# Kernel tuning notes

Measured on AMD Instinct MI355X. Metric: run time of the kernel, lower is better.

Reference implementation:

```python
import jax, jax.numpy as jnp
import numpy as np

B, T, C = 2, 2048, 1024
N_HEAD = 16
HEAD_DIM = C // N_HEAD


def setup_inputs() -> dict:
    key = jax.random.key(0)
    k1, k2, k3, k4, k5 = jax.random.split(key, 5)
    s = 1.0 / np.sqrt(C)
    return {
        "x": jax.random.normal(k1, (B, T, C), dtype=jnp.float32),
        "w_attn": jax.random.normal(k2, (C, 3 * C), dtype=jnp.float32) * s,
        "b_attn": jax.random.normal(k3, (3 * C,), dtype=jnp.float32) * 0.02,
        "w_proj": jax.random.normal(k4, (C, C), dtype=jnp.float32) * s,
        "b_proj": jax.random.normal(k5, (C,), dtype=jnp.float32) * 0.02,
    }


def reference(x, w_attn, b_attn, w_proj, b_proj):
    Bx, Tx, Cx = x.shape
    qkv = x @ w_attn + b_attn  # [B, T, 3C]
    q, k, v = jnp.split(qkv, 3, axis=2)
    # [B, H, T, D]
    q = q.reshape(Bx, Tx, N_HEAD, HEAD_DIM).transpose(0, 2, 1, 3)
    k = k.reshape(Bx, Tx, N_HEAD, HEAD_DIM).transpose(0, 2, 1, 3)
    v = v.reshape(Bx, Tx, N_HEAD, HEAD_DIM).transpose(0, 2, 1, 3)
    scale = 1.0 / jnp.sqrt(jnp.asarray(HEAD_DIM, dtype=x.dtype))
    att = jnp.einsum("bhqd,bhkd->bhqk", q, k) * scale  # [B,H,T,T]
    causal = jnp.tril(jnp.ones((Tx, Tx), dtype=bool))
    att = jnp.where(causal[None, None, :, :], att, -jnp.inf)
    att = jax.nn.softmax(att, axis=-1)
    y = jnp.einsum("bhqk,bhkd->bhqd", att, v)  # [B,H,T,D]
    y = y.transpose(0, 2, 1, 3).reshape(Bx, Tx, Cx)
    return y @ w_proj + b_proj
```

## Files before the change

### kernel.cpp

```cpp
#include <hip/hip_runtime.h>
#include <hip/hip_bf16.h>
#include <stdint.h>

#define TT 2048
#define CC 1024
#define NH 16
#define HD 64
#define BT 4096

typedef float f32x4 __attribute__((ext_vector_type(4)));
typedef __bf16 bf16x8 __attribute__((ext_vector_type(8)));
typedef __bf16 bf16x4 __attribute__((ext_vector_type(4)));

#define MFMA(a, b, c) __builtin_amdgcn_mfma_f32_16x16x32_bf16((a), (b), (c), 0, 0, 0)

__device__ __forceinline__ void gload16(const void* g, void* l) {
    __builtin_amdgcn_global_load_lds(
        (const __attribute__((address_space(1))) void*)g,
        (__attribute__((address_space(3))) void*)l,
        16, 0, 0);
}

__global__ __launch_bounds__(256) void conv_f32_bf16(
    const float* __restrict__ in, __bf16* __restrict__ out, int n4) {
    int i = blockIdx.x * blockDim.x + threadIdx.x;
    int stride = gridDim.x * blockDim.x;
    for (; i < n4; i += stride) {
        float4 v = reinterpret_cast<const float4*>(in)[i];
        bf16x4 o;
        o.x = (__bf16)v.x; o.y = (__bf16)v.y; o.z = (__bf16)v.z; o.w = (__bf16)v.w;
        reinterpret_cast<bf16x4*>(out)[i] = o;
    }
}

__global__ __launch_bounds__(256) void transpose_f32_bf16(
    const float* __restrict__ in, __bf16* __restrict__ out, int R, int C) {
    __shared__ float tile[32][33];
    int c0 = blockIdx.x * 32, r0 = blockIdx.y * 32;
    int tx = threadIdx.x, ty = threadIdx.y;
#pragma unroll
    for (int j = 0; j < 32; j += 8)
        tile[ty + j][tx] = in[(size_t)(r0 + ty + j) * C + c0 + tx];
    __syncthreads();
#pragma unroll
    for (int j = 0; j < 32; j += 8)
        out[(size_t)(c0 + ty + j) * R + r0 + tx] = (__bf16)tile[tx][ty + j];
}

template <int MODE>
__global__ __launch_bounds__(256) void gemm128(
    const __bf16* __restrict__ A, const __bf16* __restrict__ Bt,
    const float* __restrict__ bias,
    __bf16* __restrict__ oq, __bf16* __restrict__ ok, __bf16* __restrict__ ov,
    float* __restrict__ of, int M, int N, int K) {
    __shared__ __align__(16) __bf16 As[128 * 64];
    __shared__ __align__(16) __bf16 Bs[128 * 64];
    const int tid = threadIdx.x;
    const int w = tid >> 6, lane = tid & 63;
    const int l15 = lane & 15, lg = lane >> 4;
    const int m0 = blockIdx.y * 128, n0 = blockIdx.x * 128;
    const int wr = w >> 1, wc = w & 1;

    const f32x4 zero4 = {0.f, 0.f, 0.f, 0.f};
    f32x4 acc[4][4];
#pragma unroll
    for (int m = 0; m < 4; ++m)
#pragma unroll
        for (int n = 0; n < 4; ++n) acc[m][n] = zero4;

    const char* Ab = (const char*)A;
    const char* Bb = (const char*)Bt;
    const size_t rowbytes = (size_t)K * 2;

    for (int kt = 0; kt < K; kt += 64) {
#pragma unroll
        for (int j = 0; j < 4; ++j) {
            int base = (w * 4 + j) * 1024;
            int d0 = base + lane * 16;
            int row = d0 >> 7;
            int colb = d0 & 127;
            int scolb = colb ^ ((row & 7) << 4);
            gload16(Ab + (size_t)(m0 + row) * rowbytes + (size_t)kt * 2 + scolb,
                    (char*)As + base);
            gload16(Bb + (size_t)(n0 + row) * rowbytes + (size_t)kt * 2 + scolb,
                    (char*)Bs + base);
        }
        __syncthreads();
#pragma unroll
        for (int kk = 0; kk < 2; ++kk) {
            bf16x8 af[4], bfr[4];
#pragma unroll
            for (int m = 0; m < 4; ++m) {
                int row = wr * 64 + m * 16 + l15;
                int colb = kk * 64 + lg * 16;
                af[m] = *(const bf16x8*)((const char*)As + row * 128 +
                                         (colb ^ ((row & 7) << 4)));
            }
#pragma unroll
            for (int n = 0; n < 4; ++n) {
                int row = wc * 64 + n * 16 + l15;
                int colb = kk * 64 + lg * 16;
                bfr[n] = *(const bf16x8*)((const char*)Bs + row * 128 +
                                          (colb ^ ((row & 7) << 4)));
            }
#pragma unroll
            for (int m = 0; m < 4; ++m)
#pragma unroll
                for (int n = 0; n < 4; ++n)
                    acc[m][n] = MFMA(af[m], bfr[n], acc[m][n]);
        }
        __syncthreads();
    }

#pragma unroll
    for (int n = 0; n < 4; ++n) {
        int col = n0 + wc * 64 + n * 16 + l15;
        float bs = bias[col];
        if constexpr (MODE == 0) {
            int sec = col >> 10;
            int cc = col & 1023;
            int h = cc >> 6, d = cc & 63;
            if (sec == 2) {
#pragma unroll
                for (int m = 0; m < 4; ++m) {
                    int rowb = m0 + wr * 64 + m * 16 + lg * 4;
                    int bb = rowb >> 11, t = rowb & 2047;
                    bf16x4 pk;
#pragma unroll
                    for (int r = 0; r < 4; ++r) pk[r] = (__bf16)(acc[m][n][r] + bs);
                    *(bf16x4*)&ov[((size_t)(bb * NH + h) * HD + d) * TT + t] = pk;
                }
            } else {
                __bf16* dst = (sec == 0) ? oq : ok;
                float mult = (sec == 0) ? 0.125f * 1.44269504088896340736f : 1.0f;
#pragma unroll
                for (int m = 0; m < 4; ++m) {
                    int rowb = m0 + wr * 64 + m * 16 + lg * 4;
#pragma unroll
                    for (int r = 0; r < 4; ++r) {
                        int row = rowb + r;
                        int bb = row >> 11, t = row & 2047;
                        float val = (acc[m][n][r] + bs) * mult;
                        dst[((size_t)(bb * NH + h) * TT + t) * HD + d] = (__bf16)val;
                    }
                }
            }
        } else {
#pragma unroll
            for (int m = 0; m < 4; ++m) {
                int rowb = m0 + wr * 64 + m * 16 + lg * 4;
#pragma unroll
                for (int r = 0; r < 4; ++r) {
                    int row = rowb + r;
                    of[(size_t)row * N + col] = acc[m][n][r] + bs;
                }
            }
        }
    }
}

__global__ __launch_bounds__(256) void attn_kernel(
    const __bf16* __restrict__ q, const __bf16* __restrict__ k,
    const __bf16* __restrict__ vt, __bf16* __restrict__ y) {
    __shared__ __align__(16) __bf16 Kb[2][64 * 64];
    __shared__ __align__(16) __bf16 Vb[2][64 * 64];
    __shared__ __align__(16) __bf16 Pl[4][16 * 72];

    const int bh = blockIdx.y;
    const int qp = blockIdx.x;
    const int tid = threadIdx.x, w = tid >> 6, lane = tid & 63;
    const int l15 = lane & 15, lg = lane >> 4;
    const char* kh = (const char*)(k + (size_t)bh * TT * HD);
    const char* vh = (const char*)(vt + (size_t)bh * HD * TT);
    const __bf16* qh = q + (size_t)bh * TT * HD;
    const int qtA = qp, qtB = 31 - qp;
    const int nA = qtA + 1, ntot = nA + (qtB + 1);

    const f32x4 zero4 = {0.f, 0.f, 0.f, 0.f};
    float mrun, lrun;
    f32x4 oacc[4];
    bf16x8 qf[2];
    int qbw = 0;

    auto stage = [&](int kvb, int buf) {
#pragma unroll
        for (int j = 0; j < 2; ++j) {
            int d0 = ((w * 2 + j) * 64 + lane) * 16;
            int row = d0 >> 7, colb = d0 & 127;
            int scolb = colb ^ ((row & 7) << 4);
            gload16(kh + (size_t)(kvb + row) * 128 + scolb, (char*)Kb[buf] + d0);
            gload16(vh + (size_t)row * (TT * 2) + (size_t)kvb * 2 + scolb,
                    (char*)Vb[buf] + d0);
        }
    };

    auto initQ = [&](int qt) {
        qbw = qt * 64 + w * 16;
#pragma unroll
        for (int kk = 0; kk < 2; ++kk)
            qf[kk] = *(const bf16x8*)&qh[(size_t)(qbw + l15) * HD + kk * 32 + lg * 8];
        mrun = -1e30f; lrun = 0.f;
#pragma unroll
        for (int f = 0; f < 4; ++f) oacc[f] = zero4;
    };

    auto writeO = [&]() {
        const int b = bh >> 4, h = bh & 15;
        float inv = 1.0f / lrun;
#pragma unroll
        for (int f = 0; f < 4; ++f) {
            bf16x4 pk;
#pragma unroll
            for (int r = 0; r < 4; ++r) pk[r] = (__bf16)(oacc[f][r] * inv);
            *(bf16x4*)&y[(size_t)(b * TT + qbw + l15) * CC + h * 64 + f * 16 +
                         lg * 4] = pk;
        }
    };

    stage(0, 0);
    initQ(qtA);
    __syncthreads();

    for (int g = 0; g < ntot; ++g) {
        const int cur = g & 1;
        if (g + 1 < ntot)
            stage((g + 1 < nA ? g + 1 : g + 1 - nA) * 64, cur ^ 1);
        const int kb = (g < nA ? g : g - nA) * 64;

        f32x4 s[4];
#pragma unroll
        for (int kf = 0; kf < 4; ++kf) s[kf] = zero4;
        __builtin_amdgcn_s_setprio(1);
#pragma unroll
        for (int kf = 0; kf < 4; ++kf) {
            int krow = kf * 16 + l15;
            const char* kr = (const char*)Kb[cur] + krow * 128;
            bf16x8 k0 = *(const bf16x8*)(kr + ((lg * 16) ^ ((krow & 7) << 4)));
            bf16x8 k1 = *(const bf16x8*)(kr + ((64 + lg * 16) ^ ((krow & 7) << 4)));
            s[kf] = MFMA(k0, qf[0], s[kf]);
            s[kf] = MFMA(k1, qf[1], s[kf]);
        }
        __builtin_amdgcn_s_setprio(0);
        const int qq = qbw + l15;
        if (kb + 63 > qbw) {
#pragma unroll
            for (int kf = 0; kf < 4; ++kf)
#pragma unroll
                for (int r = 0; r < 4; ++r) {
                    int kk_ = kb + kf * 16 + lg * 4 + r;
                    if (kk_ > qq) s[kf][r] = -1e30f;
                }
        }
        f32x4 m01, m23;
#pragma unroll
        for (int r = 0; r < 4; ++r) {
            m01[r] = fmaxf(s[0][r], s[1][r]);
            m23[r] = fmaxf(s[2][r], s[3][r]);
        }
        float m_ = fmaxf(fmaxf(fmaxf(m01[0], m01[1]), fmaxf(m01[2], m01[3])),
                         fmaxf(fmaxf(m23[0], m23[1]), fmaxf(m23[2], m23[3])));
        m_ = fmaxf(m_, __shfl_xor(m_, 16));
        m_ = fmaxf(m_, __shfl_xor(m_, 32));
        float mn = fmaxf(mrun, m_);
        float fac = exp2f(mrun - mn);
        mrun = mn;
        float ss = 0.f;
#pragma unroll
        for (int kf = 0; kf < 4; ++kf)
#pragma unroll
            for (int r = 0; r < 4; ++r) {
                float p = exp2f(s[kf][r] - mn);
                s[kf][r] = p;
                ss += p;
            }
        ss += __shfl_xor(ss, 16);
        ss += __shfl_xor(ss, 32);
        lrun = lrun * fac + ss;
#pragma unroll
        for (int f = 0; f < 4; ++f)
#pragma unroll
            for (int r = 0; r < 4; ++r) oacc[f][r] *= fac;
#pragma unroll
        for (int kf = 0; kf < 4; ++kf) {
            bf16x4 pk;
#pragma unroll
            for (int r = 0; r < 4; ++r) pk[r] = (__bf16)s[kf][r];
            *(bf16x4*)&Pl[w][l15 * 72 + kf * 16 + lg * 4] = pk;
        }
        __builtin_amdgcn_s_setprio(1);
#pragma unroll
        for (int kq = 0; kq < 2; ++kq) {
            bf16x8 pfrag = *(const bf16x8*)&Pl[w][l15 * 72 + kq * 32 + lg * 8];
#pragma unroll
            for (int f = 0; f < 4; ++f) {
                int vrow = f * 16 + l15;
                bf16x8 vf = *(const bf16x8*)((const char*)Vb[cur] + vrow * 128 +
                                ((kq * 64 + lg * 16) ^ ((vrow & 7) << 4)));
                oacc[f] = MFMA(vf, pfrag, oacc[f]);
            }
        }
        __builtin_amdgcn_s_setprio(0);
        __syncthreads();
        if (g == nA - 1) { writeO(); initQ(qtB); }
    }
    writeO();
}

extern "C" void kernel_launch(void* const* d_in, const int* in_sizes, int n_in,
                              void* d_out, int out_size, void* d_ws, size_t ws_size,
                              hipStream_t stream) {
    const float* x      = (const float*)d_in[0];
    const float* w_attn = (const float*)d_in[1];
    const float* b_attn = (const float*)d_in[2];
    const float* w_proj = (const float*)d_in[3];
    const float* b_proj = (const float*)d_in[4];
    float* out = (float*)d_out;

    char* ws = (char*)d_ws;
    size_t off = 0;
    auto alloc = [&](size_t bytes) {
        char* p = ws + off;
        off += (bytes + 255) & ~(size_t)255;
        return p;
    };
    __bf16* xb   = (__bf16*)alloc((size_t)BT * CC * 2);
    __bf16* watb = (__bf16*)alloc((size_t)3 * CC * CC * 2);
    __bf16* wptb = (__bf16*)alloc((size_t)CC * CC * 2);
    __bf16* qb   = (__bf16*)alloc((size_t)BT * CC * 2);
    __bf16* kbuf = (__bf16*)alloc((size_t)BT * CC * 2);
    __bf16* vtb  = (__bf16*)alloc((size_t)BT * CC * 2);
    __bf16* yb   = (__bf16*)alloc((size_t)BT * CC * 2);

    conv_f32_bf16<<<1024, 256, 0, stream>>>(x, xb, BT * CC / 4);
    transpose_f32_bf16<<<dim3(3 * CC / 32, CC / 32), dim3(32, 8), 0, stream>>>(
        w_attn, watb, CC, 3 * CC);
    transpose_f32_bf16<<<dim3(CC / 32, CC / 32), dim3(32, 8), 0, stream>>>(
        w_proj, wptb, CC, CC);

    gemm128<0><<<dim3(3 * CC / 128, BT / 128), 256, 0, stream>>>(
        xb, watb, b_attn, qb, kbuf, vtb, nullptr, BT, 3 * CC, CC);

    attn_kernel<<<dim3(16, 2 * NH), 256, 0, stream>>>(qb, kbuf, vtb, yb);

    gemm128<1><<<dim3(CC / 128, BT / 128), 256, 0, stream>>>(
        yb, wptb, b_proj, nullptr, nullptr, nullptr, out, BT, CC, CC);
}
```

Measured before the change: 127.9 us.

## Triple-buffer attention K/V loads with fine-grained vmcnt waits and remap blocks

Moves the attention kernel's K/V staging from double to triple buffering, issuing loads two tiles ahead and waiting with explicit s_waitcnt vmcnt counts plus a raw s_barrier instead of __syncthreads. This is meant to hide global-memory latency better. The grid becomes 1D and is remapped so consecutive blocks cover different (batch, head) pairs, which may spread load across XCDs and caches. The P scratch row stride also drops from 72 to 68. The changes raise LDS use and depend on hand-counted vmcnt values being correct.

```diff
diff --git a/kernel.cpp b/kernel.cpp
--- a/kernel.cpp
+++ b/kernel.cpp
@@ -162,19 +162,20 @@
 __global__ __launch_bounds__(256) void attn_kernel(
     const __bf16* __restrict__ q, const __bf16* __restrict__ k,
     const __bf16* __restrict__ vt, __bf16* __restrict__ y) {
-    __shared__ __align__(16) __bf16 Kb[2][64 * 64];
-    __shared__ __align__(16) __bf16 Vb[2][64 * 64];
-    __shared__ __align__(16) __bf16 Pl[4][16 * 72];
-
-    const int bh = blockIdx.y;
-    const int qp = blockIdx.x;
+    __shared__ __align__(16) __bf16 Kb[3][64 * 64];
+    __shared__ __align__(16) __bf16 Vb[3][64 * 64];
+    __shared__ __align__(16) __bf16 Pl[4][16 * 68];
+
+    const int n = blockIdx.x;
+    const int bh = (n & 7) * 4 + ((n >> 3) & 3);
+    const int qp = n >> 5;
     const int tid = threadIdx.x, w = tid >> 6, lane = tid & 63;
     const int l15 = lane & 15, lg = lane >> 4;
     const char* kh = (const char*)(k + (size_t)bh * TT * HD);
     const char* vh = (const char*)(vt + (size_t)bh * HD * TT);
     const __bf16* qh = q + (size_t)bh * TT * HD;
     const int qtA = qp, qtB = 31 - qp;
-    const int nA = qtA + 1, ntot = nA + (qtB + 1);
+    const int nA = qtA + 1;
 
     const f32x4 zero4 = {0.f, 0.f, 0.f, 0.f};
     float mrun, lrun;
@@ -193,6 +194,7 @@
                     (char*)Vb[buf] + d0);
         }
     };
+    auto ktile = [&](int g) { return (g < nA ? g : g - nA) * 64; };
 
     auto initQ = [&](int qt) {
         qbw = qt * 64 + w * 16;
@@ -217,15 +219,17 @@
         }
     };
 
-    stage(0, 0);
+    stage(ktile(0), 0);
+    stage(ktile(1), 1);
     initQ(qtA);
-    __syncthreads();
-
-    for (int g = 0; g < ntot; ++g) {
-        const int cur = g & 1;
-        if (g + 1 < ntot)
-            stage((g + 1 < nA ? g + 1 : g + 1 - nA) * 64, cur ^ 1);
-        const int kb = (g < nA ? g : g - nA) * 64;
+    asm volatile("s_waitcnt vmcnt(4)" ::: "memory");
+    __builtin_amdgcn_sched_barrier(0);
+    __builtin_amdgcn_s_barrier();
+
+    for (int g = 0; g < 33; ++g) {
+        const int cur = g % 3;
+        if (g + 2 < 33) stage(ktile(g + 2), (g + 2) % 3);
+        const int kb = ktile(g);
 
         f32x4 s[4];
 #pragma unroll
@@ -285,12 +289,12 @@
             bf16x4 pk;
 #pragma unroll
             for (int r = 0; r < 4; ++r) pk[r] = (__bf16)s[kf][r];
-            *(bf16x4*)&Pl[w][l15 * 72 + kf * 16 + lg * 4] = pk;
+            *(bf16x4*)&Pl[w][l15 * 68 + kf * 16 + lg * 4] = pk;
         }
         __builtin_amdgcn_s_setprio(1);
 #pragma unroll
         for (int kq = 0; kq < 2; ++kq) {
-            bf16x8 pfrag = *(const bf16x8*)&Pl[w][l15 * 72 + kq * 32 + lg * 8];
+            bf16x8 pfrag = *(const bf16x8*)&Pl[w][l15 * 68 + kq * 32 + lg * 8];
 #pragma unroll
             for (int f = 0; f < 4; ++f) {
                 int vrow = f * 16 + l15;
@@ -300,7 +304,13 @@
             }
         }
         __builtin_amdgcn_s_setprio(0);
-        __syncthreads();
+
+        if (g + 1 < 33) {
+            if (g + 2 < 33) asm volatile("s_waitcnt vmcnt(4)" ::: "memory");
+            else            asm volatile("s_waitcnt vmcnt(0)" ::: "memory");
+            __builtin_amdgcn_sched_barrier(0);
+        }
+        __builtin_amdgcn_s_barrier();
         if (g == nA - 1) { writeO(); initQ(qtB); }
     }
     writeO();
@@ -340,7 +350,7 @@
     gemm128<0><<<dim3(3 * CC / 128, BT / 128), 256, 0, stream>>>(
         xb, watb, b_attn, qb, kbuf, vtb, nullptr, BT, 3 * CC, CC);
 
-    attn_kernel<<<dim3(16, 2 * NH), 256, 0, stream>>>(qb, kbuf, vtb, yb);
+    attn_kernel<<<512, 256, 0, stream>>>(qb, kbuf, vtb, yb);
 
     gemm128<1><<<dim3(CC / 128, BT / 128), 256, 0, stream>>>(
         yb, wptb, b_proj, nullptr, nullptr, nullptr, out, BT, CC, CC);
```

Result: faster. 123.4 us (-3.5%).

## Split attention into one block per query tile with longest-first scheduling

Applied to the files above, without the earlier changes.

Replaces paired query tiles per block (512 blocks, each doing qp and 31-qp) with 1024 blocks, each handling one query tile. Tiles are ordered longest first, and heads are interleaved in the block index so they spread across XCDs/L2. It also skips the rescale when the running max does not change, defers the row-sum shuffle reduction to the end, and changes the P tile padding from 72 to 68. This trades balanced per-block work for more blocks and dynamic load balancing. It risks tail imbalance and extra K/V loading for short tiles.

```diff
diff --git a/kernel.cpp b/kernel.cpp
--- a/kernel.cpp
+++ b/kernel.cpp
@@ -164,23 +164,27 @@
     const __bf16* __restrict__ vt, __bf16* __restrict__ y) {
     __shared__ __align__(16) __bf16 Kb[2][64 * 64];
     __shared__ __align__(16) __bf16 Vb[2][64 * 64];
-    __shared__ __align__(16) __bf16 Pl[4][16 * 72];
-
-    const int bh = blockIdx.y;
-    const int qp = blockIdx.x;
+    __shared__ __align__(16) __bf16 Pl[4][16 * 68];
+
+    const int n = blockIdx.x;
+    const int qt = 31 - (n >> 5);
+    const int bh = ((n & 7) << 2) | ((n >> 3) & 3);
     const int tid = threadIdx.x, w = tid >> 6, lane = tid & 63;
     const int l15 = lane & 15, lg = lane >> 4;
     const char* kh = (const char*)(k + (size_t)bh * TT * HD);
     const char* vh = (const char*)(vt + (size_t)bh * HD * TT);
     const __bf16* qh = q + (size_t)bh * TT * HD;
-    const int qtA = qp, qtB = 31 - qp;
-    const int nA = qtA + 1, ntot = nA + (qtB + 1);
+    const int qbw = qt * 64 + w * 16;
 
     const f32x4 zero4 = {0.f, 0.f, 0.f, 0.f};
-    float mrun, lrun;
+    float mrun = -1e30f, lrun = 0.f;
     f32x4 oacc[4];
     bf16x8 qf[2];
-    int qbw = 0;
+#pragma unroll
+    for (int f = 0; f < 4; ++f) oacc[f] = zero4;
+#pragma unroll
+    for (int kk = 0; kk < 2; ++kk)
+        qf[kk] = *(const bf16x8*)&qh[(size_t)(qbw + l15) * HD + kk * 32 + lg * 8];
 
     auto stage = [&](int kvb, int buf) {
 #pragma unroll
@@ -194,38 +198,13 @@
         }
     };
 
-    auto initQ = [&](int qt) {
-        qbw = qt * 64 + w * 16;
-#pragma unroll
-        for (int kk = 0; kk < 2; ++kk)
-            qf[kk] = *(const bf16x8*)&qh[(size_t)(qbw + l15) * HD + kk * 32 + lg * 8];
-        mrun = -1e30f; lrun = 0.f;
-#pragma unroll
-        for (int f = 0; f < 4; ++f) oacc[f] = zero4;
-    };
-
-    auto writeO = [&]() {
-        const int b = bh >> 4, h = bh & 15;
-        float inv = 1.0f / lrun;
-#pragma unroll
-        for (int f = 0; f < 4; ++f) {
-            bf16x4 pk;
-#pragma unroll
-            for (int r = 0; r < 4; ++r) pk[r] = (__bf16)(oacc[f][r] * inv);
-            *(bf16x4*)&y[(size_t)(b * TT + qbw + l15) * CC + h * 64 + f * 16 +
-                         lg * 4] = pk;
-        }
-    };
-
     stage(0, 0);
-    initQ(qtA);
     __syncthreads();
 
-    for (int g = 0; g < ntot; ++g) {
+    for (int g = 0; g <= qt; ++g) {
         const int cur = g & 1;
-        if (g + 1 < ntot)
-            stage((g + 1 < nA ? g + 1 : g + 1 - nA) * 64, cur ^ 1);
-        const int kb = (g < nA ? g : g - nA) * 64;
+        if (g < qt) stage((g + 1) * 64, cur ^ 1);
+        const int kb = g * 64;
 
         f32x4 s[4];
 #pragma unroll
@@ -241,8 +220,8 @@
             s[kf] = MFMA(k1, qf[1], s[kf]);
         }
         __builtin_amdgcn_s_setprio(0);
-        const int qq = qbw + l15;
-        if (kb + 63 > qbw) {
+        if (g == qt) {
+            const int qq = qbw + l15;
 #pragma unroll
             for (int kf = 0; kf < 4; ++kf)
 #pragma unroll
@@ -261,36 +240,37 @@
                          fmaxf(fmaxf(m23[0], m23[1]), fmaxf(m23[2], m23[3])));
         m_ = fmaxf(m_, __shfl_xor(m_, 16));
         m_ = fmaxf(m_, __shfl_xor(m_, 32));
-        float mn = fmaxf(mrun, m_);
-        float fac = exp2f(mrun - mn);
-        mrun = mn;
+        if (!__all(m_ <= mrun)) {
+            float mn = fmaxf(mrun, m_);
+            float fac = exp2f(mrun - mn);
+            mrun = mn;
+            lrun *= fac;
+#pragma unroll
+            for (int f = 0; f < 4; ++f)
+#pragma unroll
+                for (int r = 0; r < 4; ++r) oacc[f][r] *= fac;
+        }
         float ss = 0.f;
 #pragma unroll
         for (int kf = 0; kf < 4; ++kf)
 #pragma unroll
             for (int r = 0; r < 4; ++r) {
-                float p = exp2f(s[kf][r] - mn);
+                float p = exp2f(s[kf][r] - mrun);
                 s[kf][r] = p;
                 ss += p;
             }
-        ss += __shfl_xor(ss, 16);
-        ss += __shfl_xor(ss, 32);
-        lrun = lrun * fac + ss;
-#pragma unroll
-        for (int f = 0; f < 4; ++f)
-#pragma unroll
-            for (int r = 0; r < 4; ++r) oacc[f][r] *= fac;
+        lrun += ss;
 #pragma unroll
         for (int kf = 0; kf < 4; ++kf) {
             bf16x4 pk;
 #pragma unroll
             for (int r = 0; r < 4; ++r) pk[r] = (__bf16)s[kf][r];
-            *(bf16x4*)&Pl[w][l15 * 72 + kf * 16 + lg * 4] = pk;
+            *(bf16x4*)&Pl[w][l15 * 68 + kf * 16 + lg * 4] = pk;
         }
         __builtin_amdgcn_s_setprio(1);
 #pragma unroll
         for (int kq = 0; kq < 2; ++kq) {
-            bf16x8 pfrag = *(const bf16x8*)&Pl[w][l15 * 72 + kq * 32 + lg * 8];
+            bf16x8 pfrag = *(const bf16x8*)&Pl[w][l15 * 68 + kq * 32 + lg * 8];
 #pragma unroll
             for (int f = 0; f < 4; ++f) {
                 int vrow = f * 16 + l15;
@@ -301,9 +281,20 @@
         }
         __builtin_amdgcn_s_setprio(0);
         __syncthreads();
-        if (g == nA - 1) { writeO(); initQ(qtB); }
-    }
-    writeO();
+    }
+
+    lrun += __shfl_xor(lrun, 16);
+    lrun += __shfl_xor(lrun, 32);
+    const int b = bh >> 4, h = bh & 15;
+    float inv = 1.0f / lrun;
+#pragma unroll
+    for (int f = 0; f < 4; ++f) {
+        bf16x4 pk;
+#pragma unroll
+        for (int r = 0; r < 4; ++r) pk[r] = (__bf16)(oacc[f][r] * inv);
+        *(bf16x4*)&y[(size_t)(b * TT + qbw + l15) * CC + h * 64 + f * 16 +
+                     lg * 4] = pk;
+    }
 }
 
 extern "C" void kernel_launch(void* const* d_in, const int* in_sizes, int n_in,
@@ -340,7 +331,7 @@
     gemm128<0><<<dim3(3 * CC / 128, BT / 128), 256, 0, stream>>>(
         xb, watb, b_attn, qb, kbuf, vtb, nullptr, BT, 3 * CC, CC);
 
-    attn_kernel<<<dim3(16, 2 * NH), 256, 0, stream>>>(qb, kbuf, vtb, yb);
+    attn_kernel<<<1024, 256, 0, stream>>>(qb, kbuf, vtb, yb);
 
     gemm128<1><<<dim3(CC / 128, BT / 128), 256, 0, stream>>>(
         yb, wptb, b_proj, nullptr, nullptr, nullptr, out, BT, CC, CC);
```

Result: faster. 117.2 us (-8.3%).
